# Performance work log

Measured on AMD Instinct MI355X. Metric: run time of the kernel, lower is better.

The kernel has to match this reference:

```python
import jax, jax.numpy as jnp
import numpy as np
from jax import lax

DIM = 1024
N = 8192

def setup_inputs() -> dict:
    key = jax.random.key(0)
    ks = jax.random.split(key, 7)
    ifeats = jax.random.normal(ks[0], (N, DIM), dtype=jnp.float32)
    tfeat_n = jax.random.normal(ks[1], (1, DIM), dtype=jnp.float32)
    tfeat_a = jax.random.normal(ks[2], (1, DIM), dtype=jnp.float32)
    # Conv2d(1, 2, kernel_size=(3,5), padding=(0,2)) params, OIHW
    fan_in_c = 1 * 3 * 5
    bc = 1.0 / np.sqrt(fan_in_c)
    conv_w = jax.random.uniform(ks[3], (2, 1, 3, 5), minval=-bc, maxval=bc, dtype=jnp.float32)
    conv_b = jax.random.uniform(ks[4], (2,), minval=-bc, maxval=bc, dtype=jnp.float32)
    # Linear(2*dim, dim)
    bl = 1.0 / np.sqrt(2 * DIM)
    w2 = jax.random.uniform(ks[5], (DIM, 2 * DIM), minval=-bl, maxval=bl, dtype=jnp.float32)
    b2 = jax.random.uniform(ks[6], (DIM,), minval=-bl, maxval=bl, dtype=jnp.float32)
    return {"ifeats": ifeats, "tfeat_n": tfeat_n, "tfeat_a": tfeat_a,
            "conv_w": conv_w, "conv_b": conv_b, "w2": w2, "b2": b2}

def reference(ifeats, tfeat_n, tfeat_a, conv_w, conv_b, w2, b2):
    n, d = ifeats.shape
    # Batch the per-sample loop: feats_i = [tfeat_n; tfeat_a; ifeats[i]] -> [N,1,3,D]
    tn = jnp.broadcast_to(tfeat_n, (n, d))
    ta = jnp.broadcast_to(tfeat_a, (n, d))
    x1 = jnp.stack([tn, ta, ifeats], axis=1)[:, None]  # [N,1,3,D]
    # Conv2d(1->2, k=(3,5), pad=(0,2)): height collapses 3->1, width D preserved
    x2 = lax.conv_general_dilated(x1, conv_w, window_strides=(1, 1),
                                  padding=((0, 0), (2, 2)),
                                  dimension_numbers=("NCHW", "OIHW", "NCHW"))
    x2 = x2 + conv_b[None, :, None, None]              # [N,2,1,D]
    x2 = jax.nn.gelu(x2, approximate=False)            # torch nn.GELU() is exact
    x2 = x2.reshape(n, 2 * d)                          # channel-major flatten, matches view(1,-1)
    x3 = x2 @ w2.T + b2                                # Linear(2D -> D)
    return ifeats + x3
```

## Files before the change

### kernel.cpp

```cpp
#include <hip/hip_runtime.h>
#include <cstdint>

#define DIMD 1024
#define NROWS 8192
#define KDIM 2048

typedef unsigned short u16;
typedef __bf16 bf16x8 __attribute__((ext_vector_type(8)));
typedef float f32x4 __attribute__((ext_vector_type(4)));

__device__ __forceinline__ u16 f2bf(float f) {
  unsigned u = __builtin_bit_cast(unsigned, f);
  return (u16)((u + 0x7FFFu + ((u >> 16) & 1u)) >> 16);
}

__device__ __forceinline__ float gelu_exact(float x) {
  float s = 0.70710678118654752f * x;
  float a = fabsf(s);
  float k = __fdividef(1.0f, fmaf(0.3275911f, a, 1.0f));
  float p = 1.061405429f;
  p = fmaf(p, k, -1.453152027f);
  p = fmaf(p, k, 1.421413741f);
  p = fmaf(p, k, -0.284496736f);
  p = fmaf(p, k, 0.254829592f);
  p = p * k;
  float e = __expf(-s * s);
  float erf_s = copysignf(fmaf(-p, e, 1.0f), s);
  return 0.5f * x * (1.0f + erf_s);
}

__global__ __launch_bounds__(256) void pre_kernel(
    const float* __restrict__ ifeats, const float* __restrict__ tn,
    const float* __restrict__ ta, const float* __restrict__ cw,
    const float* __restrict__ cb, const float* __restrict__ w2,
    u16* __restrict__ x2, u16* __restrict__ w2b) {
  const int b = blockIdx.x;
  const int t = threadIdx.x;
  if (b < NROWS) {
    __shared__ float si[DIMD], sn[DIMD], sa[DIMD];
    ((float4*)si)[t] = ((const float4*)(ifeats + (size_t)b * DIMD))[t];
    ((float4*)sn)[t] = ((const float4*)tn)[t];
    ((float4*)sa)[t] = ((const float4*)ta)[t];
    __syncthreads();
    const int c = t >> 7;
    const int w0 = (t & 127) << 3;
    float cwn[5], cwa[5], cwi[5];
#pragma unroll
    for (int k = 0; k < 5; ++k) {
      cwn[k] = cw[c * 15 + k];
      cwa[k] = cw[c * 15 + 5 + k];
      cwi[k] = cw[c * 15 + 10 + k];
    }
    const float bias = cb[c];
    float wn[12], wa[12], wi[12];
#pragma unroll
    for (int j = 0; j < 12; ++j) {
      int wp = w0 - 2 + j;
      bool ok = (wp >= 0) && (wp < DIMD);
      wn[j] = ok ? sn[wp] : 0.f;
      wa[j] = ok ? sa[wp] : 0.f;
      wi[j] = ok ? si[wp] : 0.f;
    }
    union { u16 o[8]; uint4 u; } pk;
#pragma unroll
    for (int s = 0; s < 8; ++s) {
      float x = bias;
#pragma unroll
      for (int k = 0; k < 5; ++k) {
        x = fmaf(cwn[k], wn[s + k], x);
        x = fmaf(cwa[k], wa[s + k], x);
        x = fmaf(cwi[k], wi[s + k], x);
      }
      pk.o[s] = f2bf(gelu_exact(x));
    }
    *(uint4*)(x2 + (size_t)b * KDIM + c * DIMD + w0) = pk.u;
  } else {
    const int t2 = (b - NROWS) * 256 + t;
    const float4* p = (const float4*)(w2 + (size_t)t2 * 8);
    float4 a = p[0], bb = p[1];
    union { u16 o[8]; uint4 v; } pk;
    pk.o[0] = f2bf(a.x);  pk.o[1] = f2bf(a.y);  pk.o[2] = f2bf(a.z);  pk.o[3] = f2bf(a.w);
    pk.o[4] = f2bf(bb.x); pk.o[5] = f2bf(bb.y); pk.o[6] = f2bf(bb.z); pk.o[7] = f2bf(bb.w);
    *(uint4*)(w2b + (size_t)t2 * 8) = pk.v;
  }
}

__device__ __forceinline__ void gl_lds16(const u16* g, u16* l) {
  __builtin_amdgcn_global_load_lds(
      (__attribute__((address_space(1))) void*)g,
      (__attribute__((address_space(3))) void*)l, 16, 0, 0);
}

#define BK 64

__global__ __launch_bounds__(512, 4) void gemm_bt(
    const u16* __restrict__ A,
    const u16* __restrict__ B,
    const float* __restrict__ ifeats,
    const float* __restrict__ b2,
    float* __restrict__ out) {
  constexpr int K = KDIM;
  __shared__ __align__(16) u16 smem[4][128 * BK];

  const int tid = threadIdx.x;
  const int wv = tid >> 6;
  const int lane = tid & 63;
  const int kgrp = wv >> 2;
  const int wq = wv & 3;
  const int wm = (wq & 1) * 64;
  const int wn = (wq >> 1) * 64;
  const int quad = lane >> 4;
  const int r16 = lane & 15;
  const int sw = r16 & 7;
  const int poff = (((kgrp * 4 + quad) ^ sw) << 3);

  const int id = blockIdx.x;
  const int xcd = id & 7;
  const int s_ = id >> 3;
  const int i0 = (xcd * 8 + (s_ >> 3)) * 128;
  const int j0 = (s_ & 7) * 128;

  const int srow = lane >> 3;
  const int schunk = (lane & 7) ^ srow;
  const u16* gA[2];
  const u16* gB[2];
#pragma unroll
  for (int i = 0; i < 2; ++i) {
    int r = wv * 16 + i * 8 + srow;
    gA[i] = A + (size_t)(i0 + r) * K + schunk * 8;
    gB[i] = B + (size_t)(j0 + r) * K + schunk * 8;
  }

  const f32x4 vzero = {0.f, 0.f, 0.f, 0.f};
  f32x4 acc[4][4];
#pragma unroll
  for (int a = 0; a < 4; ++a)
#pragma unroll
    for (int b = 0; b < 4; ++b) acc[a][b] = vzero;

  auto stage = [&](int buf, int k0) {
#pragma unroll
    for (int i = 0; i < 2; ++i) {
      gl_lds16(gA[i] + k0, &smem[buf][(wv * 16 + i * 8) * BK]);
      gl_lds16(gB[i] + k0, &smem[2 + buf][(wv * 16 + i * 8) * BK]);
    }
  };

  auto compute = [&](int buf) {
    bf16x8 av[4], bv[4];
#pragma unroll
    for (int mt = 0; mt < 4; ++mt)
      av[mt] = *(const bf16x8*)&smem[buf][(wm + mt * 16 + r16) * BK + poff];
#pragma unroll
    for (int nt = 0; nt < 4; ++nt)
      bv[nt] = *(const bf16x8*)&smem[2 + buf][(wn + nt * 16 + r16) * BK + poff];
#pragma unroll
    for (int mt = 0; mt < 4; ++mt)
#pragma unroll
      for (int nt = 0; nt < 4; ++nt)
        acc[mt][nt] = __builtin_amdgcn_mfma_f32_16x16x32_bf16(av[mt], bv[nt], acc[mt][nt], 0, 0, 0);
  };

  stage(0, 0);
  for (int k0 = 0; k0 < K; k0 += 2 * BK) {
    __syncthreads();
    if (k0 + BK < K) stage(1, k0 + BK);
    compute(0);
    __syncthreads();
    if (k0 + 2 * BK < K) stage(0, k0 + 2 * BK);
    compute(1);
  }

  __syncthreads();
  float* scr = (float*)smem;
  if (kgrp == 1) {
#pragma unroll
    for (int nt = 0; nt < 4; ++nt)
#pragma unroll
      for (int mt = 0; mt < 4; ++mt) {
        int idx = wq * 4096 + (nt * 16 + r16) * 64 + (((mt * 4 + quad) ^ r16) << 2);
        *(f32x4*)&scr[idx] = acc[mt][nt];
      }
  }
  __syncthreads();
  if (kgrp == 0) {
#pragma unroll
    for (int nt = 0; nt < 4; ++nt) {
      int col = j0 + wn + nt * 16 + r16;
      float bias = b2[col];
#pragma unroll
      for (int mt = 0; mt < 4; ++mt) {
        int idx = wq * 4096 + (nt * 16 + r16) * 64 + (((mt * 4 + quad) ^ r16) << 2);
        f32x4 part = *(const f32x4*)&scr[idx];
        int rbase = i0 + wm + mt * 16 + quad * 4;
#pragma unroll
        for (int r = 0; r < 4; ++r) {
          size_t oix = (size_t)(rbase + r) * DIMD + col;
          out[oix] = ifeats[oix] + bias + acc[mt][nt][r] + part[r];
        }
      }
    }
  }
}

extern "C" void kernel_launch(void* const* d_in, const int* in_sizes, int n_in,
                              void* d_out, int out_size, void* d_ws, size_t ws_size,
                              hipStream_t stream) {
  const float* ifeats = (const float*)d_in[0];
  const float* tn     = (const float*)d_in[1];
  const float* ta     = (const float*)d_in[2];
  const float* cw     = (const float*)d_in[3];
  const float* cb     = (const float*)d_in[4];
  const float* w2     = (const float*)d_in[5];
  const float* b2     = (const float*)d_in[6];
  float* out = (float*)d_out;

  u16* w2b = (u16*)d_ws;
  u16* x2  = (u16*)((char*)d_ws + (size_t)DIMD * KDIM * 2);

  pre_kernel<<<NROWS + (DIMD * KDIM / 8) / 256, 256, 0, stream>>>(
      ifeats, tn, ta, cw, cb, w2, x2, w2b);
  gemm_bt<<<512, 512, 0, stream>>>(x2, w2b, ifeats, b2, out);
}
```

Before: 163.1 us.

## Split GEMM into producer/consumer warps with LDS flag synchronisation

```diff
diff --git a/kernel.cpp b/kernel.cpp
--- a/kernel.cpp
+++ b/kernel.cpp
@@ -92,6 +92,7 @@
 }
 
 #define BK 64
+#define NSTAGE (KDIM / BK)
 
 __global__ __launch_bounds__(512, 4) void gemm_bt(
     const u16* __restrict__ A,
@@ -100,36 +101,68 @@
     const float* __restrict__ b2,
     float* __restrict__ out) {
   constexpr int K = KDIM;
-  __shared__ __align__(16) u16 smem[4][128 * BK];
+  __shared__ __align__(16) u16 sA[2][128 * BK];
+  __shared__ __align__(16) u16 sB[2][128 * BK];
+  __shared__ unsigned flag_ready[2];
+  __shared__ unsigned consumed[2][4];
 
   const int tid = threadIdx.x;
   const int wv = tid >> 6;
   const int lane = tid & 63;
-  const int kgrp = wv >> 2;
-  const int wq = wv & 3;
+
+  const int id = blockIdx.x;
+  const int xcd = id & 7;
+  const int s_ = id >> 3;
+  const int i0 = (xcd * 8 + (s_ >> 3)) * 128;
+  const int j0 = (s_ & 7) * 128;
+
+  if (tid == 0) {
+    flag_ready[0] = flag_ready[1] = 0;
+#pragma unroll
+    for (int b = 0; b < 2; ++b)
+#pragma unroll
+      for (int i = 0; i < 4; ++i) consumed[b][i] = 0;
+  }
+  __syncthreads();
+
+  if (wv >= 4) {
+    const int pid = wv - 4;
+    const int lrow = lane >> 3;
+    const int gchunk = (lane & 7) ^ lrow;
+    const u16* gA = A + (size_t)(i0 + lrow) * K + gchunk * 8;
+    const u16* gB = B + (size_t)(j0 + lrow) * K + gchunk * 8;
+    for (int s = pid; s < NSTAGE; s += 4) {
+      const int b = s & 1;
+      if (s >= 2) {
+        bool ok;
+        do {
+          ok = true;
+#pragma unroll
+          for (int i = 0; i < 4; ++i)
+            ok &= (__atomic_load_n(&consumed[b][i], __ATOMIC_ACQUIRE) >=
+                   (unsigned)(s - 1));
+          if (!ok) __builtin_amdgcn_s_sleep(2);
+        } while (!ok);
+      }
+      const size_t koff = (size_t)s * BK;
+#pragma unroll
+      for (int j = 0; j < 16; ++j) {
+        gl_lds16(gA + (size_t)j * 8 * K + koff, &sA[b][j * 512]);
+        gl_lds16(gB + (size_t)j * 8 * K + koff, &sB[b][j * 512]);
+      }
+      __builtin_amdgcn_s_waitcnt(0);
+      if (lane == 0)
+        __atomic_store_n(&flag_ready[b], (unsigned)(s + 1), __ATOMIC_RELEASE);
+    }
+    return;
+  }
+
+  const int wq = wv;
   const int wm = (wq & 1) * 64;
   const int wn = (wq >> 1) * 64;
   const int quad = lane >> 4;
   const int r16 = lane & 15;
   const int sw = r16 & 7;
-  const int poff = (((kgrp * 4 + quad) ^ sw) << 3);
-
-  const int id = blockIdx.x;
-  const int xcd = id & 7;
-  const int s_ = id >> 3;
-  const int i0 = (xcd * 8 + (s_ >> 3)) * 128;
-  const int j0 = (s_ & 7) * 128;
-
-  const int srow = lane >> 3;
-  const int schunk = (lane & 7) ^ srow;
-  const u16* gA[2];
-  const u16* gB[2];
-#pragma unroll
-  for (int i = 0; i < 2; ++i) {
-    int r = wv * 16 + i * 8 + srow;
-    gA[i] = A + (size_t)(i0 + r) * K + schunk * 8;
-    gB[i] = B + (size_t)(j0 + r) * K + schunk * 8;
-  }
 
   const f32x4 vzero = {0.f, 0.f, 0.f, 0.f};
   f32x4 acc[4][4];
@@ -138,66 +171,41 @@
 #pragma unroll
     for (int b = 0; b < 4; ++b) acc[a][b] = vzero;
 
-  auto stage = [&](int buf, int k0) {
-#pragma unroll
-    for (int i = 0; i < 2; ++i) {
-      gl_lds16(gA[i] + k0, &smem[buf][(wv * 16 + i * 8) * BK]);
-      gl_lds16(gB[i] + k0, &smem[2 + buf][(wv * 16 + i * 8) * BK]);
-    }
-  };
-
-  auto compute = [&](int buf) {
-    bf16x8 av[4], bv[4];
-#pragma unroll
-    for (int mt = 0; mt < 4; ++mt)
-      av[mt] = *(const bf16x8*)&smem[buf][(wm + mt * 16 + r16) * BK + poff];
-#pragma unroll
-    for (int nt = 0; nt < 4; ++nt)
-      bv[nt] = *(const bf16x8*)&smem[2 + buf][(wn + nt * 16 + r16) * BK + poff];
-#pragma unroll
-    for (int mt = 0; mt < 4; ++mt)
+  for (int s = 0; s < NSTAGE; ++s) {
+    const int b = s & 1;
+    while (__atomic_load_n(&flag_ready[b], __ATOMIC_ACQUIRE) < (unsigned)(s + 1))
+      __builtin_amdgcn_s_sleep(1);
+#pragma unroll
+    for (int half = 0; half < 2; ++half) {
+      const int poff = (((half * 4 + quad) ^ sw) << 3);
+      bf16x8 av[4], bv[4];
+#pragma unroll
+      for (int mt = 0; mt < 4; ++mt)
+        av[mt] = *(const bf16x8*)&sA[b][(wm + mt * 16 + r16) * BK + poff];
 #pragma unroll
       for (int nt = 0; nt < 4; ++nt)
-        acc[mt][nt] = __builtin_amdgcn_mfma_f32_16x16x32_bf16(av[mt], bv[nt], acc[mt][nt], 0, 0, 0);
-  };
-
-  stage(0, 0);
-  for (int k0 = 0; k0 < K; k0 += 2 * BK) {
-    __syncthreads();
-    if (k0 + BK < K) stage(1, k0 + BK);
-    compute(0);
-    __syncthreads();
-    if (k0 + 2 * BK < K) stage(0, k0 + 2 * BK);
-    compute(1);
-  }
-
-  __syncthreads();
-  float* scr = (float*)smem;
-  if (kgrp == 1) {
-#pragma unroll
-    for (int nt = 0; nt < 4; ++nt)
-#pragma unroll
-      for (int mt = 0; mt < 4; ++mt) {
-        int idx = wq * 4096 + (nt * 16 + r16) * 64 + (((mt * 4 + quad) ^ r16) << 2);
-        *(f32x4*)&scr[idx] = acc[mt][nt];
-      }
-  }
-  __syncthreads();
-  if (kgrp == 0) {
-#pragma unroll
-    for (int nt = 0; nt < 4; ++nt) {
-      int col = j0 + wn + nt * 16 + r16;
-      float bias = b2[col];
-#pragma unroll
-      for (int mt = 0; mt < 4; ++mt) {
-        int idx = wq * 4096 + (nt * 16 + r16) * 64 + (((mt * 4 + quad) ^ r16) << 2);
-        f32x4 part = *(const f32x4*)&scr[idx];
-        int rbase = i0 + wm + mt * 16 + quad * 4;
-#pragma unroll
-        for (int r = 0; r < 4; ++r) {
-          size_t oix = (size_t)(rbase + r) * DIMD + col;
-          out[oix] = ifeats[oix] + bias + acc[mt][nt][r] + part[r];
-        }
+        bv[nt] = *(const bf16x8*)&sB[b][(wn + nt * 16 + r16) * BK + poff];
+#pragma unroll
+      for (int mt = 0; mt < 4; ++mt)
+#pragma unroll
+        for (int nt = 0; nt < 4; ++nt)
+          acc[mt][nt] = __builtin_amdgcn_mfma_f32_16x16x32_bf16(av[mt], bv[nt], acc[mt][nt], 0, 0, 0);
+    }
+    if (lane == 0)
+      __atomic_store_n(&consumed[b][wq], (unsigned)(s + 1), __ATOMIC_RELEASE);
+  }
+
+#pragma unroll
+  for (int nt = 0; nt < 4; ++nt) {
+    int col = j0 + wn + nt * 16 + r16;
+    float bias = b2[col];
+#pragma unroll
+    for (int mt = 0; mt < 4; ++mt) {
+      int rbase = i0 + wm + mt * 16 + quad * 4;
+#pragma unroll
+      for (int r = 0; r < 4; ++r) {
+        size_t oix = (size_t)(rbase + r) * DIMD + col;
+        out[oix] = ifeats[oix] + bias + acc[mt][nt][r];
       }
     }
   }
```

New measurement: 168.2 us. +3.1%, slower.
